# Optimization experiments

Hardware: AMD Instinct MI355X
Metric: run time of the kernel (lower is better)

Reference implementation:

```python
import jax, jax.numpy as jnp
import numpy as np

# Static cluster layout: B graphs, PER atoms each; first NIN are 'inside'
# (aux_ind==0), remaining NOUT are 'outside' periodic images (aux_ind==1).
B, PER, NIN, K = 256, 1024, 256, 32
NOUT = PER - NIN
N = B * PER
R = 6.0        # cutoff radius (Angstrom)
BOX = 32.0     # box side -> ~30 neighbors within R at this density


def setup_inputs() -> dict:
    key = jax.random.key(0)
    pos = jax.random.uniform(key, (N, 3), dtype=jnp.float32) * BOX
    batch = (jnp.arange(N, dtype=jnp.int32) // PER)
    aux_ind = ((jnp.arange(N, dtype=jnp.int32) % PER) >= NIN).astype(jnp.int32)
    return {"pos": pos, "batch": batch, "aux_ind": aux_ind}


def _select_neighbors(d, valid, k):
    """Pick up to k valid candidates per target, lowest candidate index first.
    d: [..., C] distances, valid: [..., C] bool. Returns (idx, mask, dist),
    each [..., k]; padded slots have mask=False and dist=0."""
    C = d.shape[-1]
    order_key = jnp.where(valid, jnp.arange(C, dtype=jnp.int32), C + 1)
    idx = jnp.argsort(order_key, axis=-1)[..., :k]          # [..., k]
    mask = jnp.take_along_axis(valid, idx, axis=-1)
    dist = jnp.where(mask, jnp.take_along_axis(d, idx, axis=-1), 0.0)
    return idx.astype(jnp.int32), mask, dist


def reference(pos, batch, aux_ind):
    # batch/aux_ind are encoded by the static contiguous layout above;
    # they parameterize the same structure torch builds via scatter_add/cumsum.
    pg = pos.reshape(B, PER, 3)
    ins = pg[:, :NIN]            # [B, NIN, 3]  inside (target + intra-conv) nodes
    outs = pg[:, NIN:]           # [B, NOUT, 3] outside (inter-conv) nodes

    # intra edges: inside -> inside, same graph, no self loops
    d_ii = jnp.sqrt(jnp.sum((ins[:, :, None, :] - ins[:, None, :, :]) ** 2, -1))  # [B,NIN,NIN]
    valid_ii = (d_ii < R) & ~jnp.eye(NIN, dtype=bool)
    idx_ii, m_ii, dist_ii = _select_neighbors(d_ii, valid_ii, K)

    # inter edges: outside -> inside, same graph
    d_io = jnp.sqrt(jnp.sum((ins[:, :, None, :] - outs[:, None, :, :]) ** 2, -1))  # [B,NIN,NOUT]
    valid_io = d_io < R
    idx_io, m_io, dist_io = _select_neighbors(d_io, valid_io, K)

    # relabel to global node indices (flow='source_to_target': row=source, col=target)
    goff = (jnp.arange(B, dtype=jnp.int32) * PER)[:, None, None]       # [B,1,1]
    tgt = jnp.broadcast_to(goff + jnp.arange(NIN, dtype=jnp.int32)[None, :, None],
                           (B, NIN, K))
    src_ii = goff + idx_ii
    src_io = goff + NIN + idx_io

    edge_index = jnp.stack([src_ii.reshape(-1), tgt.reshape(-1)], 0)        # [2, B*NIN*K]
    edge_index_inter = jnp.stack([src_io.reshape(-1), tgt.reshape(-1)], 0)  # [2, B*NIN*K]

    return (edge_index, m_ii.reshape(-1), dist_ii,
            edge_index_inter, m_io.reshape(-1), dist_io)
```

## Files before the change

kernel.cpp:

```cpp
#include <hip/hip_runtime.h>


constexpr int KK = 32;
constexpr unsigned EE = 2097152u;

typedef float v2f __attribute__((ext_vector_type(2)));

__device__ __forceinline__ v2f pk_add(v2f a, v2f b) {
    v2f d; asm("v_pk_add_f32 %0, %1, %2" : "=v"(d) : "v"(a), "v"(b)); return d;
}
__device__ __forceinline__ v2f pk_mul(v2f a, v2f b) {
    v2f d; asm("v_pk_mul_f32 %0, %1, %2" : "=v"(d) : "v"(a), "v"(b)); return d;
}

__device__ __forceinline__ int prefix_lt(unsigned long long m) {
    return __builtin_amdgcn_mbcnt_hi((unsigned)(m >> 32),
           __builtin_amdgcn_mbcnt_lo((unsigned)m, 0u));
}

__global__ __launch_bounds__(256) void mo3e_kernel(const float* __restrict__ pos,
                                                   float* __restrict__ out) {
    __shared__ float sq[3072];
    __shared__ int   slotrow[4][128];

    const int blk = blockIdx.x;
    const int b   = blk >> 6;
    const int tid = threadIdx.x;
    const int w   = tid >> 6;
    const int l   = tid & 63;
    const int i   = __builtin_amdgcn_readfirstlane(((blk & 63) << 2) | w);

    {
        const float4* g4 = (const float4*)(pos + (size_t)b * 3072);
        float4* s4 = (float4*)sq;
        s4[tid      ] = g4[tid      ];
        s4[tid + 256] = g4[tid + 256];
        s4[tid + 512] = g4[tid + 512];
    }
    __syncthreads();

    const float xi = sq[3 * i], yi = sq[3 * i + 1], zi = sq[3 * i + 2];
    const v2f nx = {-xi, -xi}, ny = {-yi, -yi}, nz = {-zi, -zi};

    int* __restrict__ row = slotrow[w];
    const int dump = 64 + l;

    unsigned long long msk[16];
    int cii = 0, cio = 0;
    int av = 3 * l;

#pragma unroll
    for (int it = 0; it < 2; ++it) {
        const float xa = sq[av], ya = sq[av + 1], za = sq[av + 2];
        const float xb = sq[av + 192], yb = sq[av + 193], zb = sq[av + 194];
        av += 384;
        const v2f qx = {xa, xb}, qy = {ya, yb}, qz = {za, zb};
        const v2f dx = pk_add(qx, nx), dy = pk_add(qy, ny), dz = pk_add(qz, nz);
        const v2f d2 = pk_add(pk_add(pk_mul(dx, dx), pk_mul(dy, dy)), pk_mul(dz, dz));
        const int c0 = it * 128;
        {
            const bool va = (d2.x < 36.0f) & ((c0 + l) != i);
            const unsigned long long m = __ballot(va);
            msk[2 * it] = m;
            int ent = cii + prefix_lt(m);
            ent = ent < 127 ? ent : 127;
            ent = va ? ent : dump;
            row[ent] = c0 + l;
            cii += __popcll(m);
        }
        {
            const bool vb = (d2.y < 36.0f) & ((c0 + 64 + l) != i);
            const unsigned long long m = __ballot(vb);
            msk[2 * it + 1] = m;
            int ent = cii + prefix_lt(m);
            ent = ent < 127 ? ent : 127;
            ent = vb ? ent : dump;
            row[ent] = c0 + 64 + l;
            cii += __popcll(m);
        }
    }
    const int S0ii = cii < KK ? cii : KK;
    if (cii < KK) {
        int pc = cii;
#pragma unroll
        for (int g = 0; g < 4; ++g) {
            const unsigned long long inv = ~msk[g];
            const bool pm = (inv >> l) & 1ull;
            int ent = pc + prefix_lt(inv);
            ent = pm ? ent : dump;
            row[ent] = g * 64 + l;
            pc += __popcll(inv);
            if (pc >= KK) break;
        }
    }

#pragma unroll
    for (int it = 2; it < 8; ++it) {
        const float xa = sq[av], ya = sq[av + 1], za = sq[av + 2];
        const float xb = sq[av + 192], yb = sq[av + 193], zb = sq[av + 194];
        av += 384;
        const v2f qx = {xa, xb}, qy = {ya, yb}, qz = {za, zb};
        const v2f dx = pk_add(qx, nx), dy = pk_add(qy, ny), dz = pk_add(qz, nz);
        const v2f d2 = pk_add(pk_add(pk_mul(dx, dx), pk_mul(dy, dy)), pk_mul(dz, dz));
        const int c0 = it * 128;
        {
            const bool va = (d2.x < 36.0f);
            const unsigned long long m = __ballot(va);
            msk[2 * it] = m;
            int ent = cio + prefix_lt(m);
            ent = ent < 95 ? ent : 95;
            ent = va ? ent + KK : dump;
            row[ent] = c0 + l;
            cio += __popcll(m);
        }
        {
            const bool vb = (d2.y < 36.0f);
            const unsigned long long m = __ballot(vb);
            msk[2 * it + 1] = m;
            int ent = cio + prefix_lt(m);
            ent = ent < 95 ? ent : 95;
            ent = vb ? ent + KK : dump;
            row[ent] = c0 + 64 + l;
            cio += __popcll(m);
        }
    }
    const int S0io = cio < KK ? cio : KK;
    if (cio < KK) {
        int pc = cio;
#pragma unroll
        for (int g = 4; g < 16; ++g) {
            const unsigned long long inv = ~msk[g];
            const bool pm = (inv >> l) & 1ull;
            int ent = pc + prefix_lt(inv);
            ent = pm ? ent + KK : dump;
            row[ent] = g * 64 + l;
            pc += __popcll(inv);
            if (pc >= KK) break;
        }
    }

    {
        const int idx = row[l];
        const float qx = sq[3 * idx], qy = sq[3 * idx + 1], qz = sq[3 * idx + 2];
        const float ddx = xi - qx, ddy = yi - qy, ddz = zi - qz;
        const float d2e = ddx * ddx + ddy * ddy + ddz * ddz;

        const bool isA = l < KK;
        const int  S0  = isA ? S0ii : S0io;
        const bool mv  = (l & 31) < S0;
        const float dist = mv ? __builtin_amdgcn_sqrtf(d2e) : 0.0f;

        const int goff = b * 1024;
        const unsigned e0  = (unsigned)(b * 256 + i) * 32u;
        const unsigned off = (isA ? 0u : 4u * EE - 32u) + e0 + (unsigned)l;

        out[off]           = (float)(goff + idx);
        out[off + EE]      = (float)(goff + i);
        out[off + 2u * EE] = mv ? 1.0f : 0.0f;
        out[off + 3u * EE] = dist;
    }
}

extern "C" void kernel_launch(void* const* d_in, const int* in_sizes, int n_in,
                              void* d_out, int out_size, void* d_ws, size_t ws_size,
                              hipStream_t stream) {
    const float* pos = (const float*)d_in[0];
    float* out = (float*)d_out;

    mo3e_kernel<<<dim3(256 * 64), dim3(256), 0, stream>>>(pos, out);
}
```

Before: 102.9 us.

## Process four targets per wave to amortize shared-memory staging of graph positions

Each wave now loops over four target atoms instead of one, and the grid shrinks from 64 to 16 blocks per graph. The aim is to cut the repeated loading of each graph's 12 KB position block into shared memory and the per-block launch overhead. The self-loop exclusion moves from a per-lane compare to clearing one bit of the ballot mask, and lane selects now use v_cndmask with an SGPR mask. In exchange, parallelism drops by 4x and each wave's work becomes serial, which could hurt latency hiding.

```diff
diff --git a/kernel.cpp b/kernel.cpp
--- a/kernel.cpp
+++ b/kernel.cpp
@@ -18,17 +18,22 @@
            __builtin_amdgcn_mbcnt_lo((unsigned)m, 0u));
 }
 
+__device__ __forceinline__ int sel_mask(int a, int b, unsigned long long m) {
+    int d; asm("v_cndmask_b32 %0, %1, %2, %3" : "=v"(d) : "v"(a), "v"(b), "s"(m));
+    return d;
+}
+
 __global__ __launch_bounds__(256) void mo3e_kernel(const float* __restrict__ pos,
                                                    float* __restrict__ out) {
     __shared__ float sq[3072];
     __shared__ int   slotrow[4][128];
 
     const int blk = blockIdx.x;
-    const int b   = blk >> 6;
+    const int b   = blk >> 4;
     const int tid = threadIdx.x;
     const int w   = tid >> 6;
     const int l   = tid & 63;
-    const int i   = __builtin_amdgcn_readfirstlane(((blk & 63) << 2) | w);
+    const int ibase = ((blk & 15) << 4) | (w << 2);
 
     {
         const float4* g4 = (const float4*)(pos + (size_t)b * 3072);
@@ -39,125 +44,122 @@
     }
     __syncthreads();
 
-    const float xi = sq[3 * i], yi = sq[3 * i + 1], zi = sq[3 * i + 2];
-    const v2f nx = {-xi, -xi}, ny = {-yi, -yi}, nz = {-zi, -zi};
-
     int* __restrict__ row = slotrow[w];
     const int dump = 64 + l;
 
-    unsigned long long msk[16];
-    int cii = 0, cio = 0;
-    int av = 3 * l;
+    for (int t = 0; t < 4; ++t) {
+        const int i = __builtin_amdgcn_readfirstlane(ibase + t);
+
+        const float xi = sq[3 * i], yi = sq[3 * i + 1], zi = sq[3 * i + 2];
+        const v2f nx = {-xi, -xi}, ny = {-yi, -yi}, nz = {-zi, -zi};
+
+        const int gself = i >> 6;
+        const unsigned long long selfclr = ~(1ull << (i & 63));
+
+        unsigned long long msk[16];
+        int cii = 0, cio = 0;
+        int av = 3 * l;
 
 #pragma unroll
-    for (int it = 0; it < 2; ++it) {
-        const float xa = sq[av], ya = sq[av + 1], za = sq[av + 2];
-        const float xb = sq[av + 192], yb = sq[av + 193], zb = sq[av + 194];
-        av += 384;
-        const v2f qx = {xa, xb}, qy = {ya, yb}, qz = {za, zb};
-        const v2f dx = pk_add(qx, nx), dy = pk_add(qy, ny), dz = pk_add(qz, nz);
-        const v2f d2 = pk_add(pk_add(pk_mul(dx, dx), pk_mul(dy, dy)), pk_mul(dz, dz));
-        const int c0 = it * 128;
-        {
-            const bool va = (d2.x < 36.0f) & ((c0 + l) != i);
-            const unsigned long long m = __ballot(va);
-            msk[2 * it] = m;
-            int ent = cii + prefix_lt(m);
-            ent = ent < 127 ? ent : 127;
-            ent = va ? ent : dump;
-            row[ent] = c0 + l;
-            cii += __popcll(m);
+        for (int it = 0; it < 2; ++it) {
+            const float xa = sq[av], ya = sq[av + 1], za = sq[av + 2];
+            const float xb = sq[av + 192], yb = sq[av + 193], zb = sq[av + 194];
+            av += 384;
+            const v2f qx = {xa, xb}, qy = {ya, yb}, qz = {za, zb};
+            const v2f dx = pk_add(qx, nx), dy = pk_add(qy, ny), dz = pk_add(qz, nz);
+            const v2f d2 = pk_add(pk_add(pk_mul(dx, dx), pk_mul(dy, dy)), pk_mul(dz, dz));
+            const int c0 = it * 128;
+            {
+                unsigned long long m = __ballot(d2.x < 36.0f);
+                if (2 * it == gself) m &= selfclr;
+                msk[2 * it] = m;
+                int ent = cii + prefix_lt(m);
+                ent = ent < 127 ? ent : 127;
+                row[sel_mask(dump, ent, m)] = c0 + l;
+                cii += __popcll(m);
+            }
+            {
+                unsigned long long m = __ballot(d2.y < 36.0f);
+                if (2 * it + 1 == gself) m &= selfclr;
+                msk[2 * it + 1] = m;
+                int ent = cii + prefix_lt(m);
+                ent = ent < 127 ? ent : 127;
+                row[sel_mask(dump, ent, m)] = c0 + 64 + l;
+                cii += __popcll(m);
+            }
         }
-        {
-            const bool vb = (d2.y < 36.0f) & ((c0 + 64 + l) != i);
-            const unsigned long long m = __ballot(vb);
-            msk[2 * it + 1] = m;
-            int ent = cii + prefix_lt(m);
-            ent = ent < 127 ? ent : 127;
-            ent = vb ? ent : dump;
-            row[ent] = c0 + 64 + l;
-            cii += __popcll(m);
+        const int S0ii = cii < KK ? cii : KK;
+        if (cii < KK) {
+            int pc = cii;
+#pragma unroll
+            for (int g = 0; g < 4; ++g) {
+                const unsigned long long inv = ~msk[g];
+                int ent = pc + prefix_lt(inv);
+                row[sel_mask(dump, ent, inv)] = g * 64 + l;
+                pc += __popcll(inv);
+                if (pc >= KK) break;
+            }
         }
-    }
-    const int S0ii = cii < KK ? cii : KK;
-    if (cii < KK) {
-        int pc = cii;
-#pragma unroll
-        for (int g = 0; g < 4; ++g) {
-            const unsigned long long inv = ~msk[g];
-            const bool pm = (inv >> l) & 1ull;
-            int ent = pc + prefix_lt(inv);
-            ent = pm ? ent : dump;
-            row[ent] = g * 64 + l;
-            pc += __popcll(inv);
-            if (pc >= KK) break;
-        }
-    }
 
 #pragma unroll
-    for (int it = 2; it < 8; ++it) {
-        const float xa = sq[av], ya = sq[av + 1], za = sq[av + 2];
-        const float xb = sq[av + 192], yb = sq[av + 193], zb = sq[av + 194];
-        av += 384;
-        const v2f qx = {xa, xb}, qy = {ya, yb}, qz = {za, zb};
-        const v2f dx = pk_add(qx, nx), dy = pk_add(qy, ny), dz = pk_add(qz, nz);
-        const v2f d2 = pk_add(pk_add(pk_mul(dx, dx), pk_mul(dy, dy)), pk_mul(dz, dz));
-        const int c0 = it * 128;
+        for (int it = 2; it < 8; ++it) {
+            const float xa = sq[av], ya = sq[av + 1], za = sq[av + 2];
+            const float xb = sq[av + 192], yb = sq[av + 193], zb = sq[av + 194];
+            av += 384;
+            const v2f qx = {xa, xb}, qy = {ya, yb}, qz = {za, zb};
+            const v2f dx = pk_add(qx, nx), dy = pk_add(qy, ny), dz = pk_add(qz, nz);
+            const v2f d2 = pk_add(pk_add(pk_mul(dx, dx), pk_mul(dy, dy)), pk_mul(dz, dz));
+            const int c0 = it * 128;
+            {
+                const unsigned long long m = __ballot(d2.x < 36.0f);
+                msk[2 * it] = m;
+                int ent = cio + prefix_lt(m);
+                ent = ent < 95 ? ent : 95;
+                row[sel_mask(dump, ent + KK, m)] = c0 + l;
+                cio += __popcll(m);
+            }
+            {
+                const unsigned long long m = __ballot(d2.y < 36.0f);
+                msk[2 * it + 1] = m;
+                int ent = cio + prefix_lt(m);
+                ent = ent < 95 ? ent : 95;
+                row[sel_mask(dump, ent + KK, m)] = c0 + 64 + l;
+                cio += __popcll(m);
+            }
+        }
+        const int S0io = cio < KK ? cio : KK;
+        if (cio < KK) {
+            int pc = cio;
+#pragma unroll
+            for (int g = 4; g < 16; ++g) {
+                const unsigned long long inv = ~msk[g];
+                int ent = pc + prefix_lt(inv);
+                row[sel_mask(dump, ent + KK, inv)] = g * 64 + l;
+                pc += __popcll(inv);
+                if (pc >= KK) break;
+            }
+        }
+
         {
-            const bool va = (d2.x < 36.0f);
-            const unsigned long long m = __ballot(va);
-            msk[2 * it] = m;
-            int ent = cio + prefix_lt(m);
-            ent = ent < 95 ? ent : 95;
-            ent = va ? ent + KK : dump;
-            row[ent] = c0 + l;
-            cio += __popcll(m);
+            const int idx = row[l];
+            const float qx = sq[3 * idx], qy = sq[3 * idx + 1], qz = sq[3 * idx + 2];
+            const float ddx = xi - qx, ddy = yi - qy, ddz = zi - qz;
+            const float d2e = ddx * ddx + ddy * ddy + ddz * ddz;
+
+            const bool isA = l < KK;
+            const int  S0  = isA ? S0ii : S0io;
+            const bool mv  = (l & 31) < S0;
+            const float dist = mv ? __builtin_amdgcn_sqrtf(d2e) : 0.0f;
+
+            const int goff = b * 1024;
+            const unsigned e0  = (unsigned)(b * 256 + i) * 32u;
+            const unsigned off = (isA ? 0u : 4u * EE - 32u) + e0 + (unsigned)l;
+
+            out[off]           = (float)(goff + idx);
+            out[off + EE]      = (float)(goff + i);
+            out[off + 2u * EE] = mv ? 1.0f : 0.0f;
+            out[off + 3u * EE] = dist;
         }
-        {
-            const bool vb = (d2.y < 36.0f);
-            const unsigned long long m = __ballot(vb);
-            msk[2 * it + 1] = m;
-            int ent = cio + prefix_lt(m);
-            ent = ent < 95 ? ent : 95;
-            ent = vb ? ent + KK : dump;
-            row[ent] = c0 + 64 + l;
-            cio += __popcll(m);
-        }
-    }
-    const int S0io = cio < KK ? cio : KK;
-    if (cio < KK) {
-        int pc = cio;
-#pragma unroll
-        for (int g = 4; g < 16; ++g) {
-            const unsigned long long inv = ~msk[g];
-            const bool pm = (inv >> l) & 1ull;
-            int ent = pc + prefix_lt(inv);
-            ent = pm ? ent + KK : dump;
-            row[ent] = g * 64 + l;
-            pc += __popcll(inv);
-            if (pc >= KK) break;
-        }
-    }
-
-    {
-        const int idx = row[l];
-        const float qx = sq[3 * idx], qy = sq[3 * idx + 1], qz = sq[3 * idx + 2];
-        const float ddx = xi - qx, ddy = yi - qy, ddz = zi - qz;
-        const float d2e = ddx * ddx + ddy * ddy + ddz * ddz;
-
-        const bool isA = l < KK;
-        const int  S0  = isA ? S0ii : S0io;
-        const bool mv  = (l & 31) < S0;
-        const float dist = mv ? __builtin_amdgcn_sqrtf(d2e) : 0.0f;
-
-        const int goff = b * 1024;
-        const unsigned e0  = (unsigned)(b * 256 + i) * 32u;
-        const unsigned off = (isA ? 0u : 4u * EE - 32u) + e0 + (unsigned)l;
-
-        out[off]           = (float)(goff + idx);
-        out[off + EE]      = (float)(goff + i);
-        out[off + 2u * EE] = mv ? 1.0f : 0.0f;
-        out[off + 3u * EE] = dist;
     }
 }
 
@@ -167,5 +169,5 @@
     const float* pos = (const float*)d_in[0];
     float* out = (float*)d_out;
 
-    mo3e_kernel<<<dim3(256 * 64), dim3(256), 0, stream>>>(pos, out);
+    mo3e_kernel<<<dim3(256 * 16), dim3(256), 0, stream>>>(pos, out);
 }
```

After: 102.6 us. Within noise of the previous version (-0.3%).
